# Kernel optimization log

Measured on AMD Instinct MI355X. Metric: run time of the kernel, lower is better.

Reference implementation:

```python
import jax, jax.numpy as jnp
import numpy as np


def setup_inputs() -> dict:
    key = jax.random.key(0)
    B, V = 2048, 32000
    input = jax.random.normal(key, (B, V), dtype=jnp.float32)
    return {"input": input}


def reference(input) -> jnp.ndarray:
    # Sparsemax along the last dim (self.dim == -1).
    x = input - jnp.max(input, axis=-1, keepdims=True)          # [B, V]
    zs = -jnp.sort(-x, axis=-1)                                  # descending sort [B, V]
    V = zs.shape[-1]
    range_values = jnp.arange(1, V + 1, dtype=x.dtype)           # [V]
    bound = 1.0 + range_values * zs                              # [B, V]
    cumsum_zs = jnp.cumsum(zs, axis=-1)                          # [B, V]
    is_gt = bound > cumsum_zs                                    # [B, V] bool
    k = jnp.sum(is_gt, axis=-1, keepdims=True).astype(x.dtype)   # [B, 1]
    k_idx = (k - 1.0).astype(jnp.int32)                          # [B, 1]
    taus = (jnp.take_along_axis(cumsum_zs, k_idx, axis=-1) - 1.0) / k  # [B, 1]
    return jnp.maximum(jnp.zeros_like(x), x - taus)
```

## Files before the change

### kernel.cpp

```cpp
#include <hip/hip_runtime.h>

#define THREADS 256
#define NWAVES (THREADS / 64)
#define CAP 2048

__global__ __launch_bounds__(THREADS) void sparsemax_kernel(
    const float* __restrict__ in, float* __restrict__ out, int V)
{
    const int row = blockIdx.x;
    const float* __restrict__ x = in + (size_t)row * V;
    float* __restrict__ y = out + (size_t)row * V;
    const int tid  = threadIdx.x;
    const int lane = tid & 63;
    const int wave = tid >> 6;

    __shared__ float s_red[NWAVES];
    __shared__ float s_cand[CAP];
    __shared__ float s_sorted[CAP];
    __shared__ int   s_count;
    __shared__ float s_m;
    __shared__ float s_tau;
    __shared__ float s_sum;

    const int V4 = V >> 2;
    const float4* __restrict__ x4 = reinterpret_cast<const float4*>(x);

    float lmax = -3.4e38f;
    for (int i = tid; i < V4; i += THREADS) {
        float4 v = x4[i];
        lmax = fmaxf(fmaxf(lmax, v.x), fmaxf(v.y, fmaxf(v.z, v.w)));
    }
    for (int i = (V4 << 2) + tid; i < V; i += THREADS)
        lmax = fmaxf(lmax, x[i]);
    #pragma unroll
    for (int off = 32; off > 0; off >>= 1)
        lmax = fmaxf(lmax, __shfl_down(lmax, off, 64));
    if (lane == 0) s_red[wave] = lmax;
    __syncthreads();
    if (tid == 0) {
        float m = s_red[0];
        for (int w = 1; w < NWAVES; ++w) m = fmaxf(m, s_red[w]);
        s_m = m;
        s_count = 0;
    }
    __syncthreads();
    const float m = s_m;

    for (int i = tid; i < V4; i += THREADS) {
        float4 v = x4[i];
        float a[4] = {v.x, v.y, v.z, v.w};
        #pragma unroll
        for (int j = 0; j < 4; ++j) {
            float z = a[j] - m;
            if (z > -1.0f) {
                int p = atomicAdd(&s_count, 1);
                if (p < CAP) s_cand[p] = z;
            }
        }
    }
    for (int i = (V4 << 2) + tid; i < V; i += THREADS) {
        float z = x[i] - m;
        if (z > -1.0f) {
            int p = atomicAdd(&s_count, 1);
            if (p < CAP) s_cand[p] = z;
        }
    }
    __syncthreads();
    const int n = s_count;

    if (n <= CAP) {
        for (int i = tid; i < n; i += THREADS) {
            float zi = s_cand[i];
            int r = 0;
            for (int j = 0; j < n; ++j) {
                float zj = s_cand[j];
                r += (zj > zi) || (zj == zi && j < i);
            }
            s_sorted[r] = zi;
        }
        __syncthreads();
        if (tid == 0) {
            float cum = 0.0f;
            int k = 0;
            for (int j = 0; j < n; ++j) {
                cum += s_sorted[j];
                if (1.0f + (float)(j + 1) * s_sorted[j] > cum) k = j + 1;
            }
            float cumk = 0.0f;
            for (int j = 0; j < k; ++j) cumk += s_sorted[j];
            s_tau = (cumk - 1.0f) / (float)k;
        }
        __syncthreads();
    } else {
        float lo = -1.0f, hi = 0.0f;
        for (int it = 0; it < 48; ++it) {
            float mid = 0.5f * (lo + hi);
            float ls = 0.0f;
            for (int i = tid; i < V4; i += THREADS) {
                float4 v = x4[i];
                ls += fmaxf(0.0f, v.x - m - mid);
                ls += fmaxf(0.0f, v.y - m - mid);
                ls += fmaxf(0.0f, v.z - m - mid);
                ls += fmaxf(0.0f, v.w - m - mid);
            }
            for (int i = (V4 << 2) + tid; i < V; i += THREADS)
                ls += fmaxf(0.0f, x[i] - m - mid);
            #pragma unroll
            for (int off = 32; off > 0; off >>= 1)
                ls += __shfl_down(ls, off, 64);
            if (lane == 0) s_red[wave] = ls;
            __syncthreads();
            if (tid == 0) {
                float s = 0.0f;
                for (int w = 0; w < NWAVES; ++w) s += s_red[w];
                s_sum = s;
            }
            __syncthreads();
            float s = s_sum;
            __syncthreads();
            if (s > 1.0f) lo = mid; else hi = mid;
        }
        if (tid == 0) s_tau = 0.5f * (lo + hi);
        __syncthreads();
    }

    const float tau = s_tau;
    const float thr = m + tau;

    float4* __restrict__ y4 = reinterpret_cast<float4*>(y);
    for (int i = tid; i < V4; i += THREADS) {
        float4 v = x4[i];
        float4 o;
        o.x = fmaxf(0.0f, v.x - thr);
        o.y = fmaxf(0.0f, v.y - thr);
        o.z = fmaxf(0.0f, v.z - thr);
        o.w = fmaxf(0.0f, v.w - thr);
        y4[i] = o;
    }
    for (int i = (V4 << 2) + tid; i < V; i += THREADS)
        y[i] = fmaxf(0.0f, x[i] - thr);
}

extern "C" void kernel_launch(void* const* d_in, const int* in_sizes, int n_in,
                              void* d_out, int out_size, void* d_ws, size_t ws_size,
                              hipStream_t stream) {
    const float* in = (const float*)d_in[0];
    float* out = (float*)d_out;
    const int V = 32000;
    const int B = in_sizes[0] / V;
    sparsemax_kernel<<<B, THREADS, 0, stream>>>(in, out, V);
}
```

Measured before the change: 512.2 us.

## Cache each row in registers with 1024-thread blocks to avoid re-reading input

Moves to 1024 threads per block, and each thread now keeps its 8 float4 of the row in registers. The max, candidate-gathering, bisection and output passes all reuse those registers instead of reloading the row from global memory. This removes two extra reads of the input per row, leaving one read and one write. In exchange it hardcodes V <= 32768 and V divisible by 4 (tail handling is dropped), raises register pressure, and may cut occupancy per CU.

```diff
diff --git a/kernel.cpp b/kernel.cpp
--- a/kernel.cpp
+++ b/kernel.cpp
@@ -1,10 +1,11 @@
 #include <hip/hip_runtime.h>
 
-#define THREADS 256
+#define THREADS 1024
 #define NWAVES (THREADS / 64)
+#define K4 8
 #define CAP 2048
 
-__global__ __launch_bounds__(THREADS) void sparsemax_kernel(
+__global__ __launch_bounds__(THREADS, 2) void sparsemax_kernel(
     const float* __restrict__ in, float* __restrict__ out, int V)
 {
     const int row = blockIdx.x;
@@ -24,14 +25,22 @@
 
     const int V4 = V >> 2;
     const float4* __restrict__ x4 = reinterpret_cast<const float4*>(x);
+    float4* __restrict__ y4 = reinterpret_cast<float4*>(y);
 
+    float4 d[K4];
     float lmax = -3.4e38f;
-    for (int i = tid; i < V4; i += THREADS) {
-        float4 v = x4[i];
-        lmax = fmaxf(fmaxf(lmax, v.x), fmaxf(v.y, fmaxf(v.z, v.w)));
+    #pragma unroll
+    for (int k = 0; k < K4; ++k) {
+        int i = k * THREADS + tid;
+        if (i < V4) {
+            float4 v = x4[i];
+            d[k] = v;
+            lmax = fmaxf(fmaxf(lmax, v.x), fmaxf(v.y, fmaxf(v.z, v.w)));
+        } else {
+            d[k] = make_float4(-3.4e38f, -3.4e38f, -3.4e38f, -3.4e38f);
+        }
     }
-    for (int i = (V4 << 2) + tid; i < V; i += THREADS)
-        lmax = fmaxf(lmax, x[i]);
+
     #pragma unroll
     for (int off = 32; off > 0; off >>= 1)
         lmax = fmaxf(lmax, __shfl_down(lmax, off, 64));
@@ -46,9 +55,9 @@
     __syncthreads();
     const float m = s_m;
 
-    for (int i = tid; i < V4; i += THREADS) {
-        float4 v = x4[i];
-        float a[4] = {v.x, v.y, v.z, v.w};
+    #pragma unroll
+    for (int k = 0; k < K4; ++k) {
+        float a[4] = {d[k].x, d[k].y, d[k].z, d[k].w};
         #pragma unroll
         for (int j = 0; j < 4; ++j) {
             float z = a[j] - m;
@@ -56,13 +65,6 @@
                 int p = atomicAdd(&s_count, 1);
                 if (p < CAP) s_cand[p] = z;
             }
-        }
-    }
-    for (int i = (V4 << 2) + tid; i < V; i += THREADS) {
-        float z = x[i] - m;
-        if (z > -1.0f) {
-            int p = atomicAdd(&s_count, 1);
-            if (p < CAP) s_cand[p] = z;
         }
     }
     __syncthreads();
@@ -96,15 +98,13 @@
         for (int it = 0; it < 48; ++it) {
             float mid = 0.5f * (lo + hi);
             float ls = 0.0f;
-            for (int i = tid; i < V4; i += THREADS) {
-                float4 v = x4[i];
-                ls += fmaxf(0.0f, v.x - m - mid);
-                ls += fmaxf(0.0f, v.y - m - mid);
-                ls += fmaxf(0.0f, v.z - m - mid);
-                ls += fmaxf(0.0f, v.w - m - mid);
+            #pragma unroll
+            for (int k = 0; k < K4; ++k) {
+                ls += fmaxf(0.0f, d[k].x - m - mid);
+                ls += fmaxf(0.0f, d[k].y - m - mid);
+                ls += fmaxf(0.0f, d[k].z - m - mid);
+                ls += fmaxf(0.0f, d[k].w - m - mid);
             }
-            for (int i = (V4 << 2) + tid; i < V; i += THREADS)
-                ls += fmaxf(0.0f, x[i] - m - mid);
             #pragma unroll
             for (int off = 32; off > 0; off >>= 1)
                 ls += __shfl_down(ls, off, 64);
@@ -124,21 +124,20 @@
         __syncthreads();
     }
 
-    const float tau = s_tau;
-    const float thr = m + tau;
+    const float thr = s_m + s_tau;
 
-    float4* __restrict__ y4 = reinterpret_cast<float4*>(y);
-    for (int i = tid; i < V4; i += THREADS) {
-        float4 v = x4[i];
-        float4 o;
-        o.x = fmaxf(0.0f, v.x - thr);
-        o.y = fmaxf(0.0f, v.y - thr);
-        o.z = fmaxf(0.0f, v.z - thr);
-        o.w = fmaxf(0.0f, v.w - thr);
-        y4[i] = o;
+    #pragma unroll
+    for (int k = 0; k < K4; ++k) {
+        int i = k * THREADS + tid;
+        if (i < V4) {
+            float4 o;
+            o.x = fmaxf(0.0f, d[k].x - thr);
+            o.y = fmaxf(0.0f, d[k].y - thr);
+            o.z = fmaxf(0.0f, d[k].z - thr);
+            o.w = fmaxf(0.0f, d[k].w - thr);
+            y4[i] = o;
+        }
     }
-    for (int i = (V4 << 2) + tid; i < V; i += THREADS)
-        y[i] = fmaxf(0.0f, x[i] - thr);
 }
 
 extern "C" void kernel_launch(void* const* d_in, const int* in_sizes, int n_in,
```

After: 446.7 us. 12.8% less time.
